# Performance work log

Measured on AMD Instinct MI355X. Metric: run time of the kernel, lower is better.

The kernel has to match this reference:

```python
import jax, jax.numpy as jnp
import numpy as np

C = 512; H = 64; W = 64; STRIDE = 16; NA = 9; IMG = 1024
PRE_NMS = 6000; POST_NMS = 300; NMS_T = 0.7; MIN_SIZE = 16.0
BBOX_CLIP = float(np.log(1000.0 / 16.0))  # standard dw/dh clamp for exp() safety


def _make_anchors():
    # 3 scales x 3 aspect ratios on a stride-16 grid -> (H*W*9, 4) xyxy anchors
    scales = np.array([128.0, 256.0, 512.0])
    ratios = np.array([0.5, 1.0, 2.0])
    hs = (scales[:, None] * np.sqrt(ratios)[None, :]).ravel()
    ws = (scales[:, None] / np.sqrt(ratios)[None, :]).ravel()
    yy, xx = np.meshgrid((np.arange(H) + 0.5) * STRIDE, (np.arange(W) + 0.5) * STRIDE, indexing='ij')
    ctr = np.stack([xx.ravel(), yy.ravel()], -1)            # (HW, 2) centers
    wh = np.stack([ws, hs], -1)                              # (9, 2)
    anc = np.concatenate([ctr[:, None, :] - 0.5 * wh[None], ctr[:, None, :] + 0.5 * wh[None]], -1)
    return anc.reshape(-1, 4).astype(np.float32)             # (HW*9, 4)


def setup_inputs() -> dict:
    key = jax.random.key(0)
    k = jax.random.split(key, 4)
    return {
        'feature_map': jax.random.normal(k[0], (1, C, H, W), jnp.float32),
        'anchors': jnp.asarray(_make_anchors()),
        'image_shape': jnp.array([IMG, IMG], jnp.int32),
        'conv1_w': 0.01 * jax.random.normal(k[1], (C, C, 3, 3), jnp.float32),
        'conv1_b': jnp.zeros((C,), jnp.float32),
        'cls_w': 0.01 * jax.random.normal(k[2], (NA, C, 1, 1), jnp.float32),
        'cls_b': jnp.zeros((NA,), jnp.float32),
        'box_w': 0.01 * jax.random.normal(k[3], (NA * 4, C, 1, 1), jnp.float32),
        'box_b': jnp.zeros((NA * 4,), jnp.float32),
    }


def _conv(x, w, b):
    dn = ('NCHW', 'OIHW', 'NCHW')
    return jax.lax.conv_general_dilated(x, w, (1, 1), 'SAME', dimension_numbers=dn) + b[None, :, None, None]


def _decode_boxes(deltas, anchors):
    aw = anchors[:, 2] - anchors[:, 0]
    ah = anchors[:, 3] - anchors[:, 1]
    ax = anchors[:, 0] + 0.5 * aw
    ay = anchors[:, 1] + 0.5 * ah
    dx, dy, dw, dh = deltas[:, 0], deltas[:, 1], deltas[:, 2], deltas[:, 3]
    dw = jnp.minimum(dw, BBOX_CLIP)
    dh = jnp.minimum(dh, BBOX_CLIP)
    px = dx * aw + ax
    py = dy * ah + ay
    pw = jnp.exp(dw) * aw
    ph = jnp.exp(dh) * ah
    return jnp.stack([px - 0.5 * pw, py - 0.5 * ph, px + 0.5 * pw, py + 0.5 * ph], -1)


def _pairwise_iou(a, b):
    area_a = (a[:, 2] - a[:, 0]) * (a[:, 3] - a[:, 1])
    area_b = (b[:, 2] - b[:, 0]) * (b[:, 3] - b[:, 1])
    lt = jnp.maximum(a[:, None, :2], b[None, :, :2])
    rb = jnp.minimum(a[:, None, 2:], b[None, :, 2:])
    wh = jnp.clip(rb - lt, 0.0)
    inter = wh[..., 0] * wh[..., 1]
    union = area_a[:, None] + area_b[None, :] - inter
    return jnp.where(union > 0, inter / union, 0.0)


def reference(feature_map, anchors, image_shape, conv1_w, conv1_b, cls_w, cls_b, box_w, box_b):
    # conv head
    y = jax.nn.relu(_conv(feature_map, conv1_w, conv1_b))
    scores = _conv(y, cls_w, cls_b).reshape(-1)            # (H*W*9,)  torch .view(-1) order
    deltas = _conv(y, box_w, box_b).reshape(-1, 4)         # (H*W*9, 4) torch .reshape(-1,4) order
    preds = _decode_boxes(deltas, anchors)

    # filter_proposals: sigmoid -> topk 6000 -> clamp -> min-size -> NMS(0.7) -> top 300
    s = jax.nn.sigmoid(scores)
    topv, topi = jax.lax.top_k(s, PRE_NMS)                  # sorted descending
    b = preds[topi]
    h_img = image_shape[0].astype(jnp.float32)
    w_img = image_shape[1].astype(jnp.float32)
    b = jnp.stack([jnp.clip(b[:, 0], 0.0, w_img), jnp.clip(b[:, 1], 0.0, h_img),
                   jnp.clip(b[:, 2], 0.0, w_img), jnp.clip(b[:, 3], 0.0, h_img)], -1)
    valid = ((b[:, 2] - b[:, 0]) >= MIN_SIZE) & ((b[:, 3] - b[:, 1]) >= MIN_SIZE)

    iou = _pairwise_iou(b, b)                               # (6000, 6000)
    idx = jnp.arange(PRE_NMS)

    def body(i, keep):  # greedy NMS in score order (boxes already sorted desc)
        sup = (iou[i] > NMS_T) & keep[i] & (idx > i)
        return keep & (~sup)

    keep = jax.lax.fori_loop(0, PRE_NMS, body, valid)
    fs = jnp.where(keep, topv, -1.0)                        # suppressed/invalid -> sentinel
    sc, i2 = jax.lax.top_k(fs, POST_NMS)
    return b[i2], sc
```

## Files before the change

kernel.cpp:

```cpp
#include <hip/hip_runtime.h>
#include <hip/hip_bf16.h>

typedef unsigned int u32;
typedef unsigned long long u64;
typedef float v2f __attribute__((ext_vector_type(2)));
typedef float v4f __attribute__((ext_vector_type(4)));

#define OFF_Y      0ull
#define OFF_WT     8388608ull
#define OFF_ZPART  8388608ull
#define OFF_SCORES 11337728ull
#define OFF_DRAW   11485184ull
#define OFF_HIST   12075008ull
#define OFF_TOPV   12665344ull
#define OFF_BOXES  12714496ull
#define OFF_VW     12812800ull
#define OFF_MASK   12813824ull

#define NS     36864
#define PRE    6000
#define POST   300
#define SORTN  8192
#define MROW   96
#define NB     32

__global__ __launch_bounds__(256) void k_wtrans(const float* __restrict__ gw,
                                                float* __restrict__ wT) {
    int o = blockIdx.x * 256 + threadIdx.x;
    if (o >= 512 * 512 * 9) return;
    int ci = o / 4608;
    int r = o - ci * 4608;
    int k = r >> 9;
    int co = r & 511;
    wT[o] = gw[co * 4608 + ci * 9 + k];
}

#define CI 16
#define XROW 66
#define CHUNK_ELEMS (CI * 3 * XROW)
#define STAGE_IT 13
__global__ __launch_bounds__(256, 4) void k_conv1(const float* __restrict__ x,
                                                  const float* __restrict__ wT,
                                                  const float* __restrict__ gb,
                                                  float* __restrict__ y) {
    __shared__ float xs[CHUNK_ELEMS];
    const int t = threadIdx.x;
    const int tx = t & 63;
    const int wv = __builtin_amdgcn_readfirstlane(t >> 6);
    const int cob = (blockIdx.x & 15) << 5;
    const int h0 = blockIdx.x >> 4;
    const int co_base = cob + (wv << 3);

    int offs[STAGE_IT];
    u32 vmask = 0;
#pragma unroll
    for (int u = 0; u < STAGE_IT; ++u) {
        int idx = t + u * 256;
        offs[u] = 0;
        if (idx < CHUNK_ELEMS) {
            int ci = idx / (3 * XROW);
            int rem = idx - ci * (3 * XROW);
            int row = rem / XROW;
            int col = rem - row * XROW;
            int gr = h0 + row - 1, gc = col - 1;
            if ((unsigned)gr < 64u && (unsigned)gc < 64u) {
                offs[u] = ci * 4096 + (gr << 6) + gc;
                vmask |= 1u << u;
            }
        }
    }

    v2f acc2[4];
#pragma unroll
    for (int j = 0; j < 4; ++j) acc2[j] = (v2f){0.f, 0.f};

    float st[STAGE_IT];
#pragma unroll
    for (int u = 0; u < STAGE_IT; ++u)
        st[u] = (vmask >> u & 1) ? x[offs[u]] : 0.f;

#pragma unroll 1
    for (int cc = 0; cc < 32; ++cc) {
        if (cc) __syncthreads();
#pragma unroll
        for (int u = 0; u < STAGE_IT; ++u) {
            int idx = t + u * 256;
            if (idx < CHUNK_ELEMS) xs[idx] = st[u];
        }
        __syncthreads();
        if (cc + 1 < 32) {
            const float* xsrc = x + (cc + 1) * CI * 4096;
#pragma unroll
            for (int u = 0; u < STAGE_IT; ++u)
                st[u] = (vmask >> u & 1) ? xsrc[offs[u]] : 0.f;
        }

        const int cig0 = cc * CI;
#pragma unroll 2
        for (int ci = 0; ci < CI; ++ci) {
            float xr[9];
            {
                const float* xp = xs + ci * (3 * XROW) + tx;
#pragma unroll
                for (int r = 0; r < 3; ++r) {
                    xr[r * 3 + 0] = xp[r * XROW + 0];
                    xr[r * 3 + 1] = xp[r * XROW + 1];
                    xr[r * 3 + 2] = xp[r * XROW + 2];
                }
            }
            const v2f* wk2 = (const v2f*)(wT + (size_t)(cig0 + ci) * 4608 + co_base);
#pragma unroll
            for (int k = 0; k < 9; ++k) {
                v2f w0 = wk2[k * 256 + 0];
                v2f w1 = wk2[k * 256 + 1];
                v2f w2 = wk2[k * 256 + 2];
                v2f w3 = wk2[k * 256 + 3];
                float xv = xr[k];
                v2f xp2 = {xv, xv};
                acc2[0] = __builtin_elementwise_fma(w0, xp2, acc2[0]);
                acc2[1] = __builtin_elementwise_fma(w1, xp2, acc2[1]);
                acc2[2] = __builtin_elementwise_fma(w2, xp2, acc2[2]);
                acc2[3] = __builtin_elementwise_fma(w3, xp2, acc2[3]);
            }
        }
    }

#pragma unroll
    for (int j = 0; j < 4; ++j) {
        int co0 = co_base + 2 * j;
        float v0 = acc2[j].x + gb[co0];
        float v1 = acc2[j].y + gb[co0 + 1];
        v0 = v0 > 0.f ? v0 : 0.f;
        v1 = v1 > 0.f ? v1 : 0.f;
        y[co0 * 4096 + (h0 << 6) + tx] = v0;
        y[(co0 + 1) * 4096 + (h0 << 6) + tx] = v1;
    }
}

__global__ __launch_bounds__(256) void k_heads_part(const float* __restrict__ y,
                                                    const float* __restrict__ cw,
                                                    const float* __restrict__ bw,
                                                    float* __restrict__ zpart,
                                                    u32* __restrict__ hist) {
    __shared__ __align__(16) float ys[64][132];
    const int t = threadIdx.x;
    {
        int hb = blockIdx.x << 9;
        hist[hb + t] = 0u;
        hist[hb + 256 + t] = 0u;
    }
    const int px = t & 63;
    const int gu = __builtin_amdgcn_readfirstlane(t >> 6);
    const int px0 = (blockIdx.x & 63) << 6;
    const int q = blockIdx.x >> 6;
    const int cib = q << 7;
    const int nch = (gu == 0) ? 12 : 11;

    const float* wrow[12];
#pragma unroll
    for (int j = 0; j < 12; ++j) {
        int ch = gu + 4 * j;
        if (ch < 9) wrow[j] = cw + ch * 512;
        else if (ch < 45) wrow[j] = bw + (ch - 9) * 512;
        else wrow[j] = cw;
    }
    float acc[12];
#pragma unroll
    for (int j = 0; j < 12; ++j) acc[j] = 0.f;

    for (int idx = t; idx < 128 * 64; idx += 256) {
        int ci = idx >> 6;
        int pp = idx & 63;
        ys[pp][ci] = y[(cib + ci) * 4096 + px0 + pp];
    }
    __syncthreads();

#pragma unroll 1
    for (int cq = 0; cq < 32; ++cq) {
        float4 yv = *(const float4*)&ys[px][cq << 2];
        float4 wv[12];
#pragma unroll
        for (int j = 0; j < 12; ++j)
            if (j < nch) wv[j] = *(const float4*)(wrow[j] + cib + (cq << 2));
#pragma unroll
        for (int j = 0; j < 12; ++j)
            if (j < nch)
                acc[j] += wv[j].x * yv.x + wv[j].y * yv.y + wv[j].z * yv.z + wv[j].w * yv.w;
    }
    for (int j = 0; j < nch; ++j) {
        int ch = gu + 4 * j;
        zpart[((q * 45 + ch) << 12) + px0 + px] = acc[j];
    }
}

__global__ __launch_bounds__(256) void k_hreduce(const float* __restrict__ zpart,
                                                 const float* __restrict__ cb,
                                                 const float* __restrict__ bb,
                                                 float* __restrict__ scores,
                                                 float* __restrict__ draw,
                                                 u32* __restrict__ hist) {
    int i = blockIdx.x * 256 + threadIdx.x;
    if (i >= 45 * 4096) return;
    int ch = i >> 12;
    int sp = i & 4095;
    float z = zpart[((0 * 45 + ch) << 12) + sp] + zpart[((1 * 45 + ch) << 12) + sp] +
              zpart[((2 * 45 + ch) << 12) + sp] + zpart[((3 * 45 + ch) << 12) + sp];
    if (ch < 9) {
        z += cb[ch];
        float s = 1.f / (1.f + expf(-z));
        scores[(ch << 12) + sp] = s;
        u32 sb = __float_as_uint(s);
        atomicAdd(&hist[sb >> 13], 1u);
    } else {
        z += bb[ch - 9];
        draw[((ch - 9) << 12) + sp] = z;
    }
}

__global__ __launch_bounds__(1024) void k_select(const u32* __restrict__ hist,
                                                 const float* __restrict__ scores,
                                                 const float* __restrict__ draw,
                                                 const float* __restrict__ anchors,
                                                 const int* __restrict__ ishape,
                                                 float* __restrict__ boxes,
                                                 float* __restrict__ topv,
                                                 u64* __restrict__ vw) {
    __shared__ u32 csum[1024];
    __shared__ u32 suf[1024];
    __shared__ u64 sk[SORTN];
    __shared__ int sel_s, cnt_s;
    const int t = threadIdx.x;

    u32 s = 0;
    {
        const uint4* hp4 = (const uint4*)(hist + t * 128);
#pragma unroll 4
        for (int i = 0; i < 32; ++i) {
            uint4 h4 = hp4[i];
            s += h4.x + h4.y + h4.z + h4.w;
        }
    }
    csum[t] = s;
    suf[t] = s;
    if (t == 0) cnt_s = 0;
    __syncthreads();
    for (int off = 1; off < 1024; off <<= 1) {
        u32 v = suf[t] + ((t + off < 1024) ? suf[t + off] : 0u);
        __syncthreads();
        suf[t] = v;
        __syncthreads();
    }
    u32 above = suf[t] - csum[t];
    if (above < (u32)PRE && suf[t] >= (u32)PRE) {
        const u32* hp = hist + t * 128;
        u32 run = above;
        int bstar = t * 128;
        u32 found = 0;
        for (int b2 = 127; b2 >= 0; --b2) {
            u32 c = hp[b2];
            if (!found && run + c >= (u32)PRE) { bstar = t * 128 + b2; found = 1; }
            if (!found) run += c;
        }
        sel_s = bstar;
    }
    for (int i = t; i < SORTN; i += 1024) sk[i] = 0;
    __syncthreads();

    const int sel = sel_s;
#pragma unroll 1
    for (int u = 0; u < 9; ++u) {
        int g = t + (u << 10);
        float4 s4 = *(const float4*)(scores + (g << 2));
#pragma unroll
        for (int e = 0; e < 4; ++e) {
            u32 sb = __float_as_uint(((const float*)&s4)[e]);
            if ((int)(sb >> 13) >= sel) {
                int p = atomicAdd(&cnt_s, 1);
                if (p < SORTN) sk[p] = ((u64)sb << 32) | (u32)(~((g << 2) + e));
            }
        }
    }
    __syncthreads();

    const int base = t << 3;
    u64 a[8];
    {
#pragma unroll
        for (int u = 0; u < 8; ++u) a[u] = sk[base + u];
#pragma unroll
        for (int k = 2; k <= 8; k <<= 1) {
#pragma unroll
            for (int j = k >> 1; j > 0; j >>= 1) {
#pragma unroll
                for (int u = 0; u < 8; ++u) {
                    if ((u & j) == 0) {
                        int l = u | j;
                        bool up = (((base + u) & k) == 0);
                        u64 x0 = a[u], x1 = a[l];
                        if (up ? (x0 < x1) : (x0 > x1)) { a[u] = x1; a[l] = x0; }
                    }
                }
            }
        }
#pragma unroll
        for (int u = 0; u < 8; ++u) sk[base + u] = a[u];
        __syncthreads();
    }
    for (int k = 16; k <= SORTN; k <<= 1) {
        for (int j = k >> 1; j >= 8; j >>= 1) {
#pragma unroll
            for (int s2 = 0; s2 < 4; ++s2) {
                int pidx = t + (s2 << 10);
                int i = ((pidx & ~(j - 1)) << 1) | (pidx & (j - 1));
                int l = i | j;
                u64 x0 = sk[i], x1 = sk[l];
                bool up = ((i & k) == 0);
                if (up ? (x0 < x1) : (x0 > x1)) { sk[i] = x1; sk[l] = x0; }
            }
            __syncthreads();
        }
#pragma unroll
        for (int u = 0; u < 8; ++u) a[u] = sk[base + u];
        {
            bool up = ((base & k) == 0);
#pragma unroll
            for (int j = 4; j > 0; j >>= 1) {
#pragma unroll
                for (int u = 0; u < 8; ++u) {
                    if ((u & j) == 0) {
                        int l = u | j;
                        u64 x0 = a[u], x1 = a[l];
                        if (up ? (x0 < x1) : (x0 > x1)) { a[u] = x1; a[l] = x0; }
                    }
                }
            }
        }
#pragma unroll
        for (int u = 0; u < 8; ++u) sk[base + u] = a[u];
        __syncthreads();
    }

    const float wimg = (float)ishape[1], himg = (float)ishape[0];
#pragma unroll 1
    for (int s2 = 0; s2 < 6; ++s2) {
        int r = (s2 << 10) + t;
        bool valid = false;
        if (r < PRE) {
            u64 key = sk[r];
            u32 sb = (u32)(key >> 32);
            int i = (int)(~(u32)key);
            topv[r] = __uint_as_float(sb);
            int c = i >> 10;
            int t4 = i & 1023;
            float4 d4 = *(const float4*)(draw + c * 4096 + (t4 << 2));
            float4 a4 = *(const float4*)(anchors + i * 4);
            float aw = a4.z - a4.x, ah = a4.w - a4.y;
            float ax = a4.x + 0.5f * aw, ay = a4.y + 0.5f * ah;
            const float CLIPV = (float)4.135166556742356;
            float dw = fminf(d4.z, CLIPV);
            float dh = fminf(d4.w, CLIPV);
            float px = d4.x * aw + ax, py = d4.y * ah + ay;
            float pw = expf(dw) * aw, ph = expf(dh) * ah;
            float x1 = fminf(fmaxf(px - 0.5f * pw, 0.f), wimg);
            float y1 = fminf(fmaxf(py - 0.5f * ph, 0.f), himg);
            float x2 = fminf(fmaxf(px + 0.5f * pw, 0.f), wimg);
            float y2 = fminf(fmaxf(py + 0.5f * ph, 0.f), himg);
            valid = (x2 - x1 >= 16.f) && (y2 - y1 >= 16.f);
            *(float4*)(boxes + r * 4) = make_float4(x1, y1, x2, y2);
        }
        u64 bm = __ballot(valid);
        if ((t & 63) == 0) vw[(s2 << 4) + (t >> 6)] = bm;
    }
}

__global__ __launch_bounds__(256) void k_mask(const float* __restrict__ boxes,
                                              u64* __restrict__ mask) {
    __shared__ float4 cbx[16 * 65];
    const int t = threadIdx.x;
    const int r0 = blockIdx.x << 4;
    const int row = r0 + (t >> 4);
    const int wloc = t & 15;
    float4 rb = *(const float4*)(boxes + row * 4);
    float area_a = (rb.z - rb.x) * (rb.w - rb.y);
    for (int chunk = 0; chunk < 6; ++chunk) {
        int j0c = chunk << 10;
        for (int idx = t; idx < 1024; idx += 256) {
            int j = j0c + idx;
            float4 v = make_float4(0.f, 0.f, 0.f, 0.f);
            if (j < PRE) v = *(const float4*)(boxes + j * 4);
            cbx[(idx >> 6) * 65 + (idx & 63)] = v;
        }
        __syncthreads();
        u64 bits = 0;
        const float4* cbr = cbx + wloc * 65;
        for (int b = 0; b < 64; ++b) {
            int j = j0c + (wloc << 6) + b;
            float4 ob = cbr[b];
            float area_b = (ob.z - ob.x) * (ob.w - ob.y);
            float ltx = fmaxf(rb.x, ob.x), lty = fmaxf(rb.y, ob.y);
            float rbx = fminf(rb.z, ob.z), rby = fminf(rb.w, ob.w);
            float wx = fmaxf(rbx - ltx, 0.f), wy = fmaxf(rby - lty, 0.f);
            float inter = wx * wy;
            float uni = area_a + area_b - inter;
            float iou = (uni > 0.f) ? (inter / uni) : 0.f;
            if (iou > 0.7f && j > row && j < PRE) bits |= (1ull << b);
        }
        mask[(size_t)row * MROW + (chunk << 4) + wloc] = bits;
        __syncthreads();
    }
}

__global__ __launch_bounds__(320) void k_nms_out(const u64* __restrict__ mask,
                                                 const u64* __restrict__ vw,
                                                 const float* __restrict__ boxes,
                                                 const float* __restrict__ topv,
                                                 float* __restrict__ out) {
    __shared__ u64 rem[MROW];
    __shared__ u64 rowsb[NB][MROW];
    __shared__ u64 kws[MROW];
    __shared__ int keepl[POST];
    const int tid = threadIdx.x;
    for (int i = tid; i < MROW; i += 320) { rem[i] = 0ull; kws[i] = 0ull; }
    __syncthreads();
    int kc = 0;
    bool done = false;
    for (int w = 0; w < 94 && !done; ++w) {
        u64 aw = vw[w] & ~rem[w];
        u64 kwbits = 0;
        while (aw != 0ull && !done) {
            int bq[NB];
            u64 tmp = aw;
#pragma unroll
            for (int q2 = 0; q2 < NB; ++q2) {
                bq[q2] = tmp ? __builtin_ctzll(tmp) : 64;
                tmp &= tmp - 1;
            }
#pragma unroll
            for (int u = 0; u < 10; ++u) {
                int i = tid + u * 320;
                if (i < NB * MROW) {
                    int q2 = i / MROW;
                    int ww = i - q2 * MROW;
                    if (bq[q2] < 64)
                        rowsb[q2][ww] = mask[(size_t)((w << 6) + bq[q2]) * MROW + ww];
                }
            }
            __syncthreads();
            for (int q2 = 0; q2 < NB; ++q2) {
                int b = bq[q2];
                if (b >= 64) break;
                if (!((aw >> b) & 1ull)) continue;
                if (tid == 0) keepl[kc] = (w << 6) + b;
                kc++;
                kwbits |= (1ull << b);
                if (kc >= POST) { done = true; break; }
                if (tid < MROW) rem[tid] |= rowsb[q2][tid];
                aw &= ~rowsb[q2][w];
                aw &= ~(1ull << b);
            }
            __syncthreads();
        }
        if (tid == 0) kws[w] = kwbits;
        __syncthreads();
    }
    __syncthreads();

    int j = tid;
    if (j >= POST) return;
    int kc2 = kc;
    int r;
    float sc;
    if (j < kc2) {
        r = keepl[j];
        sc = topv[r];
    } else {
        int target = j - kc2;
        r = PRE - 1;
        int cum = 0;
        for (int w = 0; w < 94; ++w) {
            u64 kb = kws[w];
            int nvalid = (w < 93) ? 64 : 48;
            u64 vmask2 = (nvalid == 64) ? ~0ull : ((1ull << nvalid) - 1ull);
            u64 nk = (~kb) & vmask2;
            int c = __popcll(nk);
            if (cum + c > target) {
                int need = target - cum;
                u64 m = nk;
                for (int q = 0; q < need; ++q) m &= (m - 1);
                r = (w << 6) + __builtin_ctzll(m);
                break;
            }
            cum += c;
        }
        sc = -1.0f;
    }
    out[j * 4 + 0] = boxes[r * 4 + 0];
    out[j * 4 + 1] = boxes[r * 4 + 1];
    out[j * 4 + 2] = boxes[r * 4 + 2];
    out[j * 4 + 3] = boxes[r * 4 + 3];
    out[1200 + j] = sc;
}

extern "C" void kernel_launch(void* const* d_in, const int* in_sizes, int n_in,
                              void* d_out, int out_size, void* d_ws, size_t ws_size,
                              hipStream_t stream) {
    const float* x = (const float*)d_in[0];
    const float* anchors = (const float*)d_in[1];
    const int* ishape = (const int*)d_in[2];
    const float* c1w = (const float*)d_in[3];
    const float* c1b = (const float*)d_in[4];
    const float* clw = (const float*)d_in[5];
    const float* clb = (const float*)d_in[6];
    const float* bxw = (const float*)d_in[7];
    const float* bxb = (const float*)d_in[8];

    char* ws = (char*)d_ws;
    float* y      = (float*)(ws + OFF_Y);
    float* wT     = (float*)(ws + OFF_WT);
    float* zpart  = (float*)(ws + OFF_ZPART);
    float* scores = (float*)(ws + OFF_SCORES);
    float* draw   = (float*)(ws + OFF_DRAW);
    u32*   hist   = (u32*)(ws + OFF_HIST);
    float* topv   = (float*)(ws + OFF_TOPV);
    float* boxes  = (float*)(ws + OFF_BOXES);
    u64*   vw     = (u64*)(ws + OFF_VW);
    u64*   mask   = (u64*)(ws + OFF_MASK);

    k_wtrans<<<(512 * 512 * 9 + 255) / 256, 256, 0, stream>>>(c1w, wT);
    k_conv1<<<1024, 256, 0, stream>>>(x, wT, c1b, y);
    k_heads_part<<<256, 256, 0, stream>>>(y, clw, bxw, zpart, hist);
    k_hreduce<<<(45 * 4096 + 255) / 256, 256, 0, stream>>>(zpart, clb, bxb, scores, draw, hist);
    k_select<<<1, 1024, 0, stream>>>(hist, scores, draw, anchors, ishape, boxes, topv, vw);
    k_mask<<<PRE / 16, 256, 0, stream>>>(boxes, mask);
    k_nms_out<<<1, 320, 0, stream>>>(mask, vw, boxes, topv, (float*)d_out);
}
```

Before: 731.7 us.

## Replace precomputed NMS mask with on-the-fly IoU in single-block NMS

Removes the k_mask kernel, which built the full 6000x6000 suppression bitmask, and the mask reads in the NMS kernel. Instead, a single 1024-thread block stages all boxes in shared memory and, for each kept box, computes IoU against all 6000 boxes, using ballots to OR the results into the removed-bit words. This drops the O(N^2) mask computation and its global-memory traffic in favour of about 300 serial rounds on one CU, each with a barrier and 6000 IoU evaluations.

```diff
diff --git a/kernel.cpp b/kernel.cpp
--- a/kernel.cpp
+++ b/kernel.cpp
@@ -15,14 +15,12 @@
 #define OFF_TOPV   12665344ull
 #define OFF_BOXES  12714496ull
 #define OFF_VW     12812800ull
-#define OFF_MASK   12813824ull
 
 #define NS     36864
 #define PRE    6000
 #define POST   300
 #define SORTN  8192
 #define MROW   96
-#define NB     32
 
 __global__ __launch_bounds__(256) void k_wtrans(const float* __restrict__ gw,
                                                 float* __restrict__ wT) {
@@ -373,95 +371,67 @@
     }
 }
 
-__global__ __launch_bounds__(256) void k_mask(const float* __restrict__ boxes,
-                                              u64* __restrict__ mask) {
-    __shared__ float4 cbx[16 * 65];
-    const int t = threadIdx.x;
-    const int r0 = blockIdx.x << 4;
-    const int row = r0 + (t >> 4);
-    const int wloc = t & 15;
-    float4 rb = *(const float4*)(boxes + row * 4);
-    float area_a = (rb.z - rb.x) * (rb.w - rb.y);
-    for (int chunk = 0; chunk < 6; ++chunk) {
-        int j0c = chunk << 10;
-        for (int idx = t; idx < 1024; idx += 256) {
-            int j = j0c + idx;
-            float4 v = make_float4(0.f, 0.f, 0.f, 0.f);
-            if (j < PRE) v = *(const float4*)(boxes + j * 4);
-            cbx[(idx >> 6) * 65 + (idx & 63)] = v;
-        }
-        __syncthreads();
-        u64 bits = 0;
-        const float4* cbr = cbx + wloc * 65;
-        for (int b = 0; b < 64; ++b) {
-            int j = j0c + (wloc << 6) + b;
-            float4 ob = cbr[b];
-            float area_b = (ob.z - ob.x) * (ob.w - ob.y);
-            float ltx = fmaxf(rb.x, ob.x), lty = fmaxf(rb.y, ob.y);
-            float rbx = fminf(rb.z, ob.z), rby = fminf(rb.w, ob.w);
-            float wx = fmaxf(rbx - ltx, 0.f), wy = fmaxf(rby - lty, 0.f);
-            float inter = wx * wy;
-            float uni = area_a + area_b - inter;
-            float iou = (uni > 0.f) ? (inter / uni) : 0.f;
-            if (iou > 0.7f && j > row && j < PRE) bits |= (1ull << b);
-        }
-        mask[(size_t)row * MROW + (chunk << 4) + wloc] = bits;
-        __syncthreads();
-    }
-}
-
-__global__ __launch_bounds__(320) void k_nms_out(const u64* __restrict__ mask,
-                                                 const u64* __restrict__ vw,
-                                                 const float* __restrict__ boxes,
-                                                 const float* __restrict__ topv,
-                                                 float* __restrict__ out) {
+__global__ __launch_bounds__(1024) void k_nms_out(const u64* __restrict__ vw,
+                                                  const float* __restrict__ boxes,
+                                                  const float* __restrict__ topv,
+                                                  float* __restrict__ out) {
+    __shared__ float4 bx[PRE];
+    __shared__ u64 vwl[MROW];
     __shared__ u64 rem[MROW];
-    __shared__ u64 rowsb[NB][MROW];
     __shared__ u64 kws[MROW];
     __shared__ int keepl[POST];
     const int tid = threadIdx.x;
-    for (int i = tid; i < MROW; i += 320) { rem[i] = 0ull; kws[i] = 0ull; }
+    const int lane = tid & 63;
+    const int wvi = tid >> 6;
+
+    for (int i = tid; i < PRE; i += 1024)
+        bx[i] = *(const float4*)(boxes + i * 4);
+    if (tid < MROW) {
+        vwl[tid] = (tid < 94) ? vw[tid] : 0ull;
+        rem[tid] = 0ull;
+        kws[tid] = 0ull;
+    }
     __syncthreads();
+
     int kc = 0;
     bool done = false;
     for (int w = 0; w < 94 && !done; ++w) {
-        u64 aw = vw[w] & ~rem[w];
+        u64 procmask = 0;
         u64 kwbits = 0;
-        while (aw != 0ull && !done) {
-            int bq[NB];
-            u64 tmp = aw;
-#pragma unroll
-            for (int q2 = 0; q2 < NB; ++q2) {
-                bq[q2] = tmp ? __builtin_ctzll(tmp) : 64;
-                tmp &= tmp - 1;
-            }
-#pragma unroll
-            for (int u = 0; u < 10; ++u) {
-                int i = tid + u * 320;
-                if (i < NB * MROW) {
-                    int q2 = i / MROW;
-                    int ww = i - q2 * MROW;
-                    if (bq[q2] < 64)
-                        rowsb[q2][ww] = mask[(size_t)((w << 6) + bq[q2]) * MROW + ww];
+        for (;;) {
+            u64 aw = vwl[w] & ~rem[w] & ~procmask;
+            if (!aw) break;
+            int b = __builtin_ctzll(aw);
+            int r = (w << 6) + b;
+            if (tid == 0) keepl[kc] = r;
+            kc++;
+            kwbits |= (1ull << b);
+            procmask |= (1ull << b);
+            if (kc >= POST) { done = true; break; }
+            float4 rb = bx[r];
+            float area_a = (rb.z - rb.x) * (rb.w - rb.y);
+#pragma unroll
+            for (int s = 0; s < 6; ++s) {
+                int j = tid + (s << 10);
+                bool sup = false;
+                if (j < PRE) {
+                    float4 ob = bx[j];
+                    float area_b = (ob.z - ob.x) * (ob.w - ob.y);
+                    float ltx = fmaxf(rb.x, ob.x), lty = fmaxf(rb.y, ob.y);
+                    float rbx = fminf(rb.z, ob.z), rby = fminf(rb.w, ob.w);
+                    float wx = fmaxf(rbx - ltx, 0.f), wy = fmaxf(rby - lty, 0.f);
+                    float inter = wx * wy;
+                    float uni = area_a + area_b - inter;
+                    float iou = (uni > 0.f) ? (inter / uni) : 0.f;
+                    sup = (iou > 0.7f) && (j > r);
                 }
+                u64 bal = __ballot(sup);
+                int widx = (s << 4) + wvi;
+                if (lane == 0 && widx < MROW) rem[widx] |= bal;
             }
             __syncthreads();
-            for (int q2 = 0; q2 < NB; ++q2) {
-                int b = bq[q2];
-                if (b >= 64) break;
-                if (!((aw >> b) & 1ull)) continue;
-                if (tid == 0) keepl[kc] = (w << 6) + b;
-                kc++;
-                kwbits |= (1ull << b);
-                if (kc >= POST) { done = true; break; }
-                if (tid < MROW) rem[tid] |= rowsb[q2][tid];
-                aw &= ~rowsb[q2][w];
-                aw &= ~(1ull << b);
-            }
-            __syncthreads();
         }
         if (tid == 0) kws[w] = kwbits;
-        __syncthreads();
     }
     __syncthreads();
 
@@ -494,10 +464,11 @@
         }
         sc = -1.0f;
     }
-    out[j * 4 + 0] = boxes[r * 4 + 0];
-    out[j * 4 + 1] = boxes[r * 4 + 1];
-    out[j * 4 + 2] = boxes[r * 4 + 2];
-    out[j * 4 + 3] = boxes[r * 4 + 3];
+    float4 ob = bx[r];
+    out[j * 4 + 0] = ob.x;
+    out[j * 4 + 1] = ob.y;
+    out[j * 4 + 2] = ob.z;
+    out[j * 4 + 3] = ob.w;
     out[1200 + j] = sc;
 }
 
@@ -524,13 +495,11 @@
     float* topv   = (float*)(ws + OFF_TOPV);
     float* boxes  = (float*)(ws + OFF_BOXES);
     u64*   vw     = (u64*)(ws + OFF_VW);
-    u64*   mask   = (u64*)(ws + OFF_MASK);
 
     k_wtrans<<<(512 * 512 * 9 + 255) / 256, 256, 0, stream>>>(c1w, wT);
     k_conv1<<<1024, 256, 0, stream>>>(x, wT, c1b, y);
     k_heads_part<<<256, 256, 0, stream>>>(y, clw, bxw, zpart, hist);
     k_hreduce<<<(45 * 4096 + 255) / 256, 256, 0, stream>>>(zpart, clb, bxb, scores, draw, hist);
     k_select<<<1, 1024, 0, stream>>>(hist, scores, draw, anchors, ishape, boxes, topv, vw);
-    k_mask<<<PRE / 16, 256, 0, stream>>>(boxes, mask);
-    k_nms_out<<<1, 320, 0, stream>>>(mask, vw, boxes, topv, (float*)d_out);
-}
+    k_nms_out<<<1, 1024, 0, stream>>>(vw, boxes, topv, (float*)d_out);
+}
```

Measured after the change: 1.059 ms. +44.7%, slower.

## Run greedy NMS scan in a single wavefront with register-held suppression state

Applied to the files above, without the earlier changes.

The serial NMS reduction now runs in one 64-lane wavefront. The removed-bits and valid-bits words stay in registers and are exchanged with cross-lane shuffles, replacing the shared-memory arrays and block-wide barriers. Candidate mask rows are fetched 8 at a time straight into registers instead of 32 at a time through shared memory. This removes __syncthreads on the sequential critical path, at the cost of more, smaller batched global loads and less load parallelism per step.

```diff
diff --git a/kernel.cpp b/kernel.cpp
--- a/kernel.cpp
+++ b/kernel.cpp
@@ -22,7 +22,7 @@
 #define POST   300
 #define SORTN  8192
 #define MROW   96
-#define NB     32
+#define NBW    8
 
 __global__ __launch_bounds__(256) void k_wtrans(const float* __restrict__ gw,
                                                 float* __restrict__ wT) {
@@ -410,64 +410,78 @@
     }
 }
 
+__device__ __forceinline__ u64 shfl64(u64 v, int src) {
+    u32 lo = __shfl((u32)v, src, 64);
+    u32 hi = __shfl((u32)(v >> 32), src, 64);
+    return ((u64)hi << 32) | lo;
+}
 __global__ __launch_bounds__(320) void k_nms_out(const u64* __restrict__ mask,
                                                  const u64* __restrict__ vw,
                                                  const float* __restrict__ boxes,
                                                  const float* __restrict__ topv,
                                                  float* __restrict__ out) {
-    __shared__ u64 rem[MROW];
-    __shared__ u64 rowsb[NB][MROW];
     __shared__ u64 kws[MROW];
     __shared__ int keepl[POST];
+    __shared__ int kc_s;
     const int tid = threadIdx.x;
-    for (int i = tid; i < MROW; i += 320) { rem[i] = 0ull; kws[i] = 0ull; }
+    if (tid < MROW) kws[tid] = 0ull;
     __syncthreads();
-    int kc = 0;
-    bool done = false;
-    for (int w = 0; w < 94 && !done; ++w) {
-        u64 aw = vw[w] & ~rem[w];
-        u64 kwbits = 0;
-        while (aw != 0ull && !done) {
-            int bq[NB];
-            u64 tmp = aw;
-#pragma unroll
-            for (int q2 = 0; q2 < NB; ++q2) {
-                bq[q2] = tmp ? __builtin_ctzll(tmp) : 64;
-                tmp &= tmp - 1;
-            }
-#pragma unroll
-            for (int u = 0; u < 10; ++u) {
-                int i = tid + u * 320;
-                if (i < NB * MROW) {
-                    int q2 = i / MROW;
-                    int ww = i - q2 * MROW;
-                    if (bq[q2] < 64)
-                        rowsb[q2][ww] = mask[(size_t)((w << 6) + bq[q2]) * MROW + ww];
+
+    if (tid < 64) {
+        const int lane = tid;
+        u64 vw0 = (lane < 94) ? vw[lane] : 0ull;
+        u64 vw1 = (lane < 30) ? vw[64 + lane] : 0ull;
+        u64 rem0 = 0ull, rem1 = 0ull;
+        int kc = 0;
+        bool done = false;
+        for (int w = 0; w < 94 && !done; ++w) {
+            u64 vww  = (w < 64) ? shfl64(vw0, w)  : shfl64(vw1, w - 64);
+            u64 remw = (w < 64) ? shfl64(rem0, w) : shfl64(rem1, w - 64);
+            u64 aw = vww & ~remw;
+            u64 kwbits = 0;
+            while (aw && !done) {
+                int bq[NBW];
+                u64 tmp = aw;
+#pragma unroll
+                for (int q = 0; q < NBW; ++q) {
+                    bq[q] = tmp ? __builtin_ctzll(tmp) : 64;
+                    tmp &= tmp - 1;
                 }
-            }
-            __syncthreads();
-            for (int q2 = 0; q2 < NB; ++q2) {
-                int b = bq[q2];
-                if (b >= 64) break;
-                if (!((aw >> b) & 1ull)) continue;
-                if (tid == 0) keepl[kc] = (w << 6) + b;
-                kc++;
-                kwbits |= (1ull << b);
-                if (kc >= POST) { done = true; break; }
-                if (tid < MROW) rem[tid] |= rowsb[q2][tid];
-                aw &= ~rowsb[q2][w];
-                aw &= ~(1ull << b);
-            }
-            __syncthreads();
-        }
-        if (tid == 0) kws[w] = kwbits;
-        __syncthreads();
+                u64 rq0[NBW], rq1[NBW];
+#pragma unroll
+                for (int q = 0; q < NBW; ++q) {
+                    rq0[q] = 0ull; rq1[q] = 0ull;
+                    if (bq[q] < 64) {
+                        const u64* mrow = mask + (size_t)((w << 6) + bq[q]) * MROW;
+                        rq0[q] = mrow[lane];
+                        if (lane < 30) rq1[q] = mrow[64 + lane];
+                    }
+                }
+#pragma unroll
+                for (int q = 0; q < NBW; ++q) {
+                    int b = bq[q];
+                    if (b >= 64) break;
+                    if (!((aw >> b) & 1ull)) continue;
+                    if (lane == 0) keepl[kc] = (w << 6) + b;
+                    kc++;
+                    kwbits |= (1ull << b);
+                    if (kc >= POST) { done = true; break; }
+                    rem0 |= rq0[q];
+                    rem1 |= rq1[q];
+                    u64 roww = (w < 64) ? shfl64(rq0[q], w) : shfl64(rq1[q], w - 64);
+                    aw &= ~roww;
+                    aw &= ~(1ull << b);
+                }
+            }
+            if (lane == 0) kws[w] = kwbits;
+        }
+        if (lane == 0) kc_s = kc;
     }
     __syncthreads();
 
     int j = tid;
     if (j >= POST) return;
-    int kc2 = kc;
+    int kc2 = kc_s;
     int r;
     float sc;
     if (j < kc2) {
```

New measurement: 672.8 us. 8.1% less time.
